# Performance work log

Measured on AMD Instinct MI355X. Metric: run time of the kernel, lower is better.

The kernel has to match this reference:

```python
import jax, jax.numpy as jnp
import numpy as np

N, D_IN, D_OUT = 4096, 1024, 1024


def setup_inputs() -> dict:
    key = jax.random.key(0)
    kx, kq, kk, kv = jax.random.split(key, 4)
    s = 1.0 / np.sqrt(D_IN)
    return {
        "x": jax.random.normal(kx, (N, D_IN), dtype=jnp.float32),
        "Wq": jax.random.normal(kq, (D_OUT, D_IN), dtype=jnp.float32) * s,
        "Wk": jax.random.normal(kk, (D_OUT, D_IN), dtype=jnp.float32) * s,
        "Wv": jax.random.normal(kv, (D_OUT, D_IN), dtype=jnp.float32) * s,
    }


def reference(x, Wq, Wk, Wv):
    # nn.Linear(d_in, d_out, bias=False): y = x @ W.T with W: [d_out, d_in]
    q = x @ Wq.T            # [N, d_out]
    k = x @ Wk.T            # [N, d_out]
    v = x @ Wv.T            # [N, d_out]
    scores = q @ k.T        # [N, N]
    scale = 1.0 / jnp.sqrt(jnp.asarray(k.shape[-1], dtype=x.dtype))
    attn = jax.nn.softmax(scores * scale, axis=-1)
    return attn @ v         # [N, d_out]
```

## Files before the change

kernel.cpp:

```cpp
#include <hip/hip_runtime.h>


typedef __attribute__((ext_vector_type(8))) __bf16 bf16x8;
typedef __attribute__((ext_vector_type(4))) float floatx4;

#define GLB_AS __attribute__((address_space(1)))
#define LDS_AS __attribute__((address_space(3)))

static __device__ __forceinline__ unsigned short f2bf_u16(float f) {
  union { float f; unsigned u; } x; x.f = f;
  unsigned r = x.u;
  r += 0x7fffu + ((r >> 16) & 1u);
  return (unsigned short)(r >> 16);
}
static __device__ __forceinline__ float bf2f(unsigned short u) {
  union { unsigned u; float f; } x; x.u = ((unsigned)u) << 16; return x.f;
}

__global__ __launch_bounds__(256) void cast_all(const float* __restrict__ x,
                                                const float* __restrict__ Wq,
                                                const float* __restrict__ Wk,
                                                const float* __restrict__ Wv,
                                                unsigned short* __restrict__ xb,
                                                unsigned short* __restrict__ wb) {
  const int i = blockIdx.x * 256 + threadIdx.x;
  const int NX4 = 4096 * 1024 / 4;
  const int NW4 = 1024 * 1024 / 4;
  const float* src; unsigned short* dst; int k;
  if (i < NX4)                { src = x;  dst = xb;                   k = i; }
  else if (i < NX4 + NW4)     { src = Wq; dst = wb;                   k = i - NX4; }
  else if (i < NX4 + 2 * NW4) { src = Wk; dst = wb + 1024 * 1024;     k = i - NX4 - NW4; }
  else                        { src = Wv; dst = wb + 2 * 1024 * 1024; k = i - NX4 - 2 * NW4; }
  float4 v = reinterpret_cast<const float4*>(src)[k];
  ushort4 o = make_ushort4(f2bf_u16(v.x), f2bf_u16(v.y), f2bf_u16(v.z), f2bf_u16(v.w));
  reinterpret_cast<ushort4*>(dst)[k] = o;
}

struct GemmOuts { void* c[4]; int ldc[4]; };

template <int EPI>
__global__ __launch_bounds__(256, 2) void gemm_bt(const unsigned short* __restrict__ A,
                                                  const unsigned short* __restrict__ B,
                                                  GemmOuts outs, int lda, int ldb,
                                                  int klen, float scale) {
  __shared__ unsigned short sh[24576];
  const int t = threadIdx.x;
  const int w = t >> 6, lane = t & 63;
  const int wm = w >> 1, wn = w & 1;
  const int gx = gridDim.x;
  const int nwg = gx * gridDim.y;
  int bid = blockIdx.y * gx + blockIdx.x;
  bid = (bid & 7) * (nwg >> 3) + (bid >> 3);
  const int row0 = (bid / gx) * 256;
  const int col0 = (bid % gx) * 128;
  const int z = blockIdx.z;
  const int kstart = z * klen;
  const int NT = klen >> 5;

  const int srow = t >> 2;
  const int scbe = (((t & 3) ^ ((t >> 3) & 3)) << 3);
  const unsigned short* gA0 = A + (size_t)(row0 + srow) * lda + kstart + scbe;
  const unsigned short* gA1 = gA0 + (size_t)64 * lda;
  const unsigned short* gA2 = gA0 + (size_t)128 * lda;
  const unsigned short* gA3 = gA0 + (size_t)192 * lda;
  const unsigned short* gB0 = B + (size_t)(col0 + srow) * ldb + kstart + scbe;
  const unsigned short* gB1 = gB0 + (size_t)64 * ldb;

#define STAGE(tl_) do { \
    const int bb_ = ((tl_) & 1) * 12288; \
    __builtin_amdgcn_global_load_lds((const GLB_AS void*)(gA0 + (tl_) * 32), \
        (LDS_AS void*)&sh[bb_ + t * 8], 16, 0, 0); \
    __builtin_amdgcn_global_load_lds((const GLB_AS void*)(gA1 + (tl_) * 32), \
        (LDS_AS void*)&sh[bb_ + 2048 + t * 8], 16, 0, 0); \
    __builtin_amdgcn_global_load_lds((const GLB_AS void*)(gA2 + (tl_) * 32), \
        (LDS_AS void*)&sh[bb_ + 4096 + t * 8], 16, 0, 0); \
    __builtin_amdgcn_global_load_lds((const GLB_AS void*)(gA3 + (tl_) * 32), \
        (LDS_AS void*)&sh[bb_ + 6144 + t * 8], 16, 0, 0); \
    __builtin_amdgcn_global_load_lds((const GLB_AS void*)(gB0 + (tl_) * 32), \
        (LDS_AS void*)&sh[bb_ + 8192 + t * 8], 16, 0, 0); \
    __builtin_amdgcn_global_load_lds((const GLB_AS void*)(gB1 + (tl_) * 32), \
        (LDS_AS void*)&sh[bb_ + 10240 + t * 8], 16, 0, 0); \
  } while (0)

  const int fr = lane & 15;
  const int sg = (((lane >> 4) ^ ((lane >> 1) & 3)) << 3);
  int aofs[8], bofs[4];
#pragma unroll
  for (int mf = 0; mf < 8; ++mf) aofs[mf] = ((wm * 128 + mf * 16 + fr) << 5) + sg;
#pragma unroll
  for (int nf = 0; nf < 4; ++nf) bofs[nf] = 8192 + ((wn * 64 + nf * 16 + fr) << 5) + sg;

  floatx4 acc[8][4] = {};

  STAGE(0);

  for (int tile = 0; tile < NT; ++tile) {
    if (tile + 1 < NT) {
      STAGE(tile + 1);
      asm volatile("s_waitcnt vmcnt(6)" ::: "memory");
    } else {
      asm volatile("s_waitcnt vmcnt(0)" ::: "memory");
    }
    __builtin_amdgcn_s_barrier();

    const int bo = (tile & 1) * 12288;
    bf16x8 af[8], bf[4];
#pragma unroll
    for (int mf = 0; mf < 8; ++mf) af[mf] = *(const bf16x8*)&sh[bo + aofs[mf]];
#pragma unroll
    for (int nf = 0; nf < 4; ++nf) bf[nf] = *(const bf16x8*)&sh[bo + bofs[nf]];
    __builtin_amdgcn_s_setprio(1);
#pragma unroll
    for (int mf = 0; mf < 8; ++mf)
#pragma unroll
      for (int nf = 0; nf < 4; ++nf)
        acc[mf][nf] = __builtin_amdgcn_mfma_f32_16x16x32_bf16(af[mf], bf[nf], acc[mf][nf], 0, 0, 0);
    __builtin_amdgcn_s_setprio(0);

    __builtin_amdgcn_s_barrier();
  }
#undef STAGE

  const int er = (lane >> 4) * 4;
  const int ec = lane & 15;

  if (EPI == 0) {
    unsigned short* Cb = (unsigned short*)outs.c[z];
    const int ldc = outs.ldc[z];
#pragma unroll
    for (int mf = 0; mf < 8; ++mf)
#pragma unroll
      for (int nf = 0; nf < 4; ++nf)
#pragma unroll
        for (int r = 0; r < 4; ++r)
          Cb[(size_t)(row0 + wm * 128 + mf * 16 + er + r) * ldc +
             (col0 + wn * 64 + nf * 16 + ec)] = f2bf_u16(acc[mf][nf][r] * scale);
  } else if (EPI == 2) {
    unsigned short* Pb = (unsigned short*)outs.c[0];
    float* rsp = (float*)outs.c[1];
    const int ldc = outs.ldc[0];
    const int rj = ((col0 >> 7) * 2 + wn) * 4096;
#pragma unroll
    for (int mf = 0; mf < 8; ++mf) {
#pragma unroll
      for (int r = 0; r < 4; ++r) {
        const int m = row0 + wm * 128 + mf * 16 + er + r;
        float rsum = 0.f;
#pragma unroll
        for (int nf = 0; nf < 4; ++nf) {
          const float e = __expf(acc[mf][nf][r] * scale);
          Pb[(size_t)m * ldc + (col0 + wn * 64 + nf * 16 + ec)] = f2bf_u16(e);
          rsum += e;
        }
        rsum += __shfl_xor(rsum, 1);
        rsum += __shfl_xor(rsum, 2);
        rsum += __shfl_xor(rsum, 4);
        rsum += __shfl_xor(rsum, 8);
        if (ec == 0) rsp[rj + m] = rsum;
      }
    }
  } else {
    if (col0 < 2048) {
      unsigned short* qkb = (unsigned short*)outs.c[0];
#pragma unroll
      for (int mf = 0; mf < 8; ++mf)
#pragma unroll
        for (int nf = 0; nf < 4; ++nf)
#pragma unroll
          for (int r = 0; r < 4; ++r)
            qkb[(size_t)(row0 + wm * 128 + mf * 16 + er + r) * 2048 +
                (col0 + wn * 64 + nf * 16 + ec)] = f2bf_u16(acc[mf][nf][r]);
    } else {
      unsigned short* vT = (unsigned short*)outs.c[1];
#pragma unroll
      for (int mf = 0; mf < 8; ++mf)
#pragma unroll
        for (int nf = 0; nf < 4; ++nf) {
          const int n = (col0 - 2048) + wn * 64 + nf * 16 + ec;
          const int mb = row0 + wm * 128 + mf * 16 + er;
          ushort4 o = make_ushort4(f2bf_u16(acc[mf][nf][0]), f2bf_u16(acc[mf][nf][1]),
                                   f2bf_u16(acc[mf][nf][2]), f2bf_u16(acc[mf][nf][3]));
          *reinterpret_cast<ushort4*>(&vT[(size_t)n * 4096 + mb]) = o;
        }
    }
  }
}

__global__ __launch_bounds__(256) void reduce_pv(float* __restrict__ out,
                                                 const unsigned short* __restrict__ p0,
                                                 const unsigned short* __restrict__ p1,
                                                 const float* __restrict__ rsp) {
  const int row = blockIdx.x;
  const int lane = threadIdx.x & 63;
  float s = rsp[lane * 4096 + row];
#pragma unroll
  for (int off = 32; off >= 1; off >>= 1) s += __shfl_xor(s, off);
  const float inv = 1.0f / s;
  const int idx = row * 256 + threadIdx.x;
  ushort4 a = ((const ushort4*)p0)[idx];
  ushort4 b = ((const ushort4*)p1)[idx];
  float4 o;
  o.x = (bf2f(a.x) + bf2f(b.x)) * inv;
  o.y = (bf2f(a.y) + bf2f(b.y)) * inv;
  o.z = (bf2f(a.z) + bf2f(b.z)) * inv;
  o.w = (bf2f(a.w) + bf2f(b.w)) * inv;
  ((float4*)out)[idx] = o;
}

extern "C" void kernel_launch(void* const* d_in, const int* in_sizes, int n_in,
                              void* d_out, int out_size, void* d_ws, size_t ws_size,
                              hipStream_t stream) {
  const float* x  = (const float*)d_in[0];
  const float* Wq = (const float*)d_in[1];
  const float* Wk = (const float*)d_in[2];
  const float* Wv = (const float*)d_in[3];
  float* out = (float*)d_out;

  const int N = 4096, D = 1024;

  char* ws = (char*)d_ws;
  unsigned short* P   = (unsigned short*)ws;
  unsigned short* qkb = (unsigned short*)(ws + (32u << 20));
  unsigned short* vT  = (unsigned short*)(ws + (48u << 20));
  unsigned short* xb  = (unsigned short*)(ws + (56u << 20));
  unsigned short* wb  = (unsigned short*)(ws + (64u << 20));
  float*          rsp = (float*)(ws + (70u << 20));
  unsigned short* p0  = xb;
  unsigned short* p1  = (unsigned short*)(ws + (72u << 20));

  cast_all<<<7168, 256, 0, stream>>>(x, Wq, Wk, Wv, xb, wb);

  GemmOuts oq; oq.c[0] = qkb; oq.c[1] = vT; oq.c[2] = oq.c[3] = qkb;
  oq.ldc[0] = 2048; oq.ldc[1] = 4096; oq.ldc[2] = oq.ldc[3] = 2048;
  gemm_bt<3><<<dim3(3 * D / 128, N / 256, 1), 256, 0, stream>>>(xb, wb, oq, D, D, D, 1.0f);

  GemmOuts os; os.c[0] = P; os.c[1] = rsp; os.c[2] = os.c[3] = P;
  os.ldc[0] = N; os.ldc[1] = 0; os.ldc[2] = os.ldc[3] = N;
  gemm_bt<2><<<dim3(N / 128, N / 256, 1), 256, 0, stream>>>(qkb, qkb + D, os, 2 * D, 2 * D, D, 0.03125f);

  GemmOuts op;
  op.c[0] = p0; op.ldc[0] = D;
  op.c[1] = p1; op.ldc[1] = D;
  op.c[2] = p0; op.ldc[2] = D;
  op.c[3] = p1; op.ldc[3] = D;
  gemm_bt<0><<<dim3(D / 128, N / 256, 2), 256, 0, stream>>>(P, vT, op, N, N, N / 2, 1.0f);

  reduce_pv<<<N, 256, 0, stream>>>(out, p0, p1, rsp);
}
```

Baseline: 141.7 us.

## Fuse fp32-to-bf16 input cast into QKV projection GEMM

Removes the separate cast kernel and has a dedicated QKV GEMM read fp32 x and weights directly, converting to bf16 with packed converts while staging into LDS. This saves a kernel launch and the write and reread of the bf16 copies of x and the weights. In exchange the GEMM reads fp32 data, twice the bytes per tile, and x is re-read and re-converted by each of the 24 column blocks. The prefetch is held in registers, which raises register pressure.

```diff
diff --git a/kernel.cpp b/kernel.cpp
--- a/kernel.cpp
+++ b/kernel.cpp
@@ -16,24 +16,10 @@
 static __device__ __forceinline__ float bf2f(unsigned short u) {
   union { unsigned u; float f; } x; x.u = ((unsigned)u) << 16; return x.f;
 }
-
-__global__ __launch_bounds__(256) void cast_all(const float* __restrict__ x,
-                                                const float* __restrict__ Wq,
-                                                const float* __restrict__ Wk,
-                                                const float* __restrict__ Wv,
-                                                unsigned short* __restrict__ xb,
-                                                unsigned short* __restrict__ wb) {
-  const int i = blockIdx.x * 256 + threadIdx.x;
-  const int NX4 = 4096 * 1024 / 4;
-  const int NW4 = 1024 * 1024 / 4;
-  const float* src; unsigned short* dst; int k;
-  if (i < NX4)                { src = x;  dst = xb;                   k = i; }
-  else if (i < NX4 + NW4)     { src = Wq; dst = wb;                   k = i - NX4; }
-  else if (i < NX4 + 2 * NW4) { src = Wk; dst = wb + 1024 * 1024;     k = i - NX4 - NW4; }
-  else                        { src = Wv; dst = wb + 2 * 1024 * 1024; k = i - NX4 - 2 * NW4; }
-  float4 v = reinterpret_cast<const float4*>(src)[k];
-  ushort4 o = make_ushort4(f2bf_u16(v.x), f2bf_u16(v.y), f2bf_u16(v.z), f2bf_u16(v.w));
-  reinterpret_cast<ushort4*>(dst)[k] = o;
+static __device__ __forceinline__ unsigned cvt_pk_bf16(float lo, float hi) {
+  unsigned r;
+  asm("v_cvt_pk_bf16_f32 %0, %1, %2" : "=v"(r) : "v"(lo), "v"(hi));
+  return r;
 }
 
 struct GemmOuts { void* c[4]; int ldc[4]; };
@@ -135,7 +121,7 @@
         for (int r = 0; r < 4; ++r)
           Cb[(size_t)(row0 + wm * 128 + mf * 16 + er + r) * ldc +
              (col0 + wn * 64 + nf * 16 + ec)] = f2bf_u16(acc[mf][nf][r] * scale);
-  } else if (EPI == 2) {
+  } else {
     unsigned short* Pb = (unsigned short*)outs.c[0];
     float* rsp = (float*)outs.c[1];
     const int ldc = outs.ldc[0];
@@ -159,30 +145,120 @@
         if (ec == 0) rsp[rj + m] = rsum;
       }
     }
+  }
+}
+
+__global__ __launch_bounds__(256, 2) void gemm_qkv(const float* __restrict__ X,
+                                                   const float* __restrict__ Wq,
+                                                   const float* __restrict__ Wk,
+                                                   const float* __restrict__ Wv,
+                                                   unsigned short* __restrict__ qkb,
+                                                   unsigned short* __restrict__ vT) {
+  __shared__ unsigned short sh[24576];
+  const int t = threadIdx.x;
+  const int w = t >> 6, lane = t & 63;
+  const int wm = w >> 1, wn = w & 1;
+  const int gx = gridDim.x;
+  const int nwg = gx * gridDim.y;
+  int bid = blockIdx.y * gx + blockIdx.x;
+  bid = (bid & 7) * (nwg >> 3) + (bid >> 3);
+  const int row0 = (bid / gx) * 256;
+  const int col0 = (bid % gx) * 128;
+  const float* Wsel = col0 < 1024 ? Wq : (col0 < 2048 ? Wk : Wv);
+  const int brow = col0 & 1023;
+  const int NT = 32;
+
+  const int srow = t >> 2;
+  const int scbe = (((t & 3) ^ ((t >> 3) & 3)) << 3);
+  const float* gA = X + (size_t)(row0 + srow) * 1024 + scbe;
+  const float* gB = Wsel + (size_t)(brow + srow) * 1024 + scbe;
+
+  float4 ra[12];
+#define LOADF(kt_) do { \
+    _Pragma("unroll") for (int r_ = 0; r_ < 4; ++r_) { \
+      const float* p_ = gA + (size_t)(r_ * 64) * 1024 + (kt_); \
+      ra[2 * r_]     = *(const float4*)p_; \
+      ra[2 * r_ + 1] = *(const float4*)(p_ + 4); } \
+    _Pragma("unroll") for (int r_ = 0; r_ < 2; ++r_) { \
+      const float* p_ = gB + (size_t)(r_ * 64) * 1024 + (kt_); \
+      ra[8 + 2 * r_] = *(const float4*)p_; \
+      ra[9 + 2 * r_] = *(const float4*)(p_ + 4); } \
+  } while (0)
+#define WRITELDS(bb_) do { \
+    _Pragma("unroll") for (int r_ = 0; r_ < 6; ++r_) { \
+      uint4 pk_; \
+      pk_.x = cvt_pk_bf16(ra[2 * r_].x,     ra[2 * r_].y); \
+      pk_.y = cvt_pk_bf16(ra[2 * r_].z,     ra[2 * r_].w); \
+      pk_.z = cvt_pk_bf16(ra[2 * r_ + 1].x, ra[2 * r_ + 1].y); \
+      pk_.w = cvt_pk_bf16(ra[2 * r_ + 1].z, ra[2 * r_ + 1].w); \
+      *(uint4*)&sh[(bb_) + r_ * 2048 + t * 8] = pk_; } \
+  } while (0)
+
+  const int fr = lane & 15;
+  const int sg = (((lane >> 4) ^ ((lane >> 1) & 3)) << 3);
+  int aofs[8], bofs[4];
+#pragma unroll
+  for (int mf = 0; mf < 8; ++mf) aofs[mf] = ((wm * 128 + mf * 16 + fr) << 5) + sg;
+#pragma unroll
+  for (int nf = 0; nf < 4; ++nf) bofs[nf] = 8192 + ((wn * 64 + nf * 16 + fr) << 5) + sg;
+
+  floatx4 acc[8][4] = {};
+
+  LOADF(0);
+  asm volatile("s_waitcnt vmcnt(0)" ::: "memory");
+  WRITELDS(0);
+  LOADF(32);
+  asm volatile("s_waitcnt lgkmcnt(0)" ::: "memory");
+  __builtin_amdgcn_s_barrier();
+
+  for (int tile = 0; tile < NT; ++tile) {
+    const int bo = (tile & 1) * 12288;
+    bf16x8 af[8], bf[4];
+#pragma unroll
+    for (int mf = 0; mf < 8; ++mf) af[mf] = *(const bf16x8*)&sh[bo + aofs[mf]];
+#pragma unroll
+    for (int nf = 0; nf < 4; ++nf) bf[nf] = *(const bf16x8*)&sh[bo + bofs[nf]];
+    __builtin_amdgcn_s_setprio(1);
+#pragma unroll
+    for (int mf = 0; mf < 8; ++mf)
+#pragma unroll
+      for (int nf = 0; nf < 4; ++nf)
+        acc[mf][nf] = __builtin_amdgcn_mfma_f32_16x16x32_bf16(af[mf], bf[nf], acc[mf][nf], 0, 0, 0);
+    __builtin_amdgcn_s_setprio(0);
+
+    if (tile + 1 < NT) {
+      asm volatile("s_waitcnt vmcnt(0)" ::: "memory");
+      WRITELDS(((tile + 1) & 1) * 12288);
+      if (tile + 2 < NT) LOADF((tile + 2) * 32);
+    }
+    asm volatile("s_waitcnt lgkmcnt(0)" ::: "memory");
+    __builtin_amdgcn_s_barrier();
+  }
+#undef LOADF
+#undef WRITELDS
+
+  const int er = (lane >> 4) * 4;
+  const int ec = lane & 15;
+  if (col0 < 2048) {
+#pragma unroll
+    for (int mf = 0; mf < 8; ++mf)
+#pragma unroll
+      for (int nf = 0; nf < 4; ++nf)
+#pragma unroll
+        for (int r = 0; r < 4; ++r)
+          qkb[(size_t)(row0 + wm * 128 + mf * 16 + er + r) * 2048 +
+              (col0 + wn * 64 + nf * 16 + ec)] = f2bf_u16(acc[mf][nf][r]);
   } else {
-    if (col0 < 2048) {
-      unsigned short* qkb = (unsigned short*)outs.c[0];
-#pragma unroll
-      for (int mf = 0; mf < 8; ++mf)
-#pragma unroll
-        for (int nf = 0; nf < 4; ++nf)
-#pragma unroll
-          for (int r = 0; r < 4; ++r)
-            qkb[(size_t)(row0 + wm * 128 + mf * 16 + er + r) * 2048 +
-                (col0 + wn * 64 + nf * 16 + ec)] = f2bf_u16(acc[mf][nf][r]);
-    } else {
-      unsigned short* vT = (unsigned short*)outs.c[1];
-#pragma unroll
-      for (int mf = 0; mf < 8; ++mf)
-#pragma unroll
-        for (int nf = 0; nf < 4; ++nf) {
-          const int n = (col0 - 2048) + wn * 64 + nf * 16 + ec;
-          const int mb = row0 + wm * 128 + mf * 16 + er;
-          ushort4 o = make_ushort4(f2bf_u16(acc[mf][nf][0]), f2bf_u16(acc[mf][nf][1]),
-                                   f2bf_u16(acc[mf][nf][2]), f2bf_u16(acc[mf][nf][3]));
-          *reinterpret_cast<ushort4*>(&vT[(size_t)n * 4096 + mb]) = o;
-        }
-    }
+#pragma unroll
+    for (int mf = 0; mf < 8; ++mf)
+#pragma unroll
+      for (int nf = 0; nf < 4; ++nf) {
+        const int n = (col0 - 2048) + wn * 64 + nf * 16 + ec;
+        const int mb = row0 + wm * 128 + mf * 16 + er;
+        ushort4 o = make_ushort4(f2bf_u16(acc[mf][nf][0]), f2bf_u16(acc[mf][nf][1]),
+                                 f2bf_u16(acc[mf][nf][2]), f2bf_u16(acc[mf][nf][3]));
+        *reinterpret_cast<ushort4*>(&vT[(size_t)n * 4096 + mb]) = o;
+      }
   }
 }
 
@@ -222,17 +298,11 @@
   unsigned short* P   = (unsigned short*)ws;
   unsigned short* qkb = (unsigned short*)(ws + (32u << 20));
   unsigned short* vT  = (unsigned short*)(ws + (48u << 20));
-  unsigned short* xb  = (unsigned short*)(ws + (56u << 20));
-  unsigned short* wb  = (unsigned short*)(ws + (64u << 20));
+  unsigned short* p0  = (unsigned short*)(ws + (56u << 20));
   float*          rsp = (float*)(ws + (70u << 20));
-  unsigned short* p0  = xb;
   unsigned short* p1  = (unsigned short*)(ws + (72u << 20));
 
-  cast_all<<<7168, 256, 0, stream>>>(x, Wq, Wk, Wv, xb, wb);
-
-  GemmOuts oq; oq.c[0] = qkb; oq.c[1] = vT; oq.c[2] = oq.c[3] = qkb;
-  oq.ldc[0] = 2048; oq.ldc[1] = 4096; oq.ldc[2] = oq.ldc[3] = 2048;
-  gemm_bt<3><<<dim3(3 * D / 128, N / 256, 1), 256, 0, stream>>>(xb, wb, oq, D, D, D, 1.0f);
+  gemm_qkv<<<dim3(3 * D / 128, N / 256, 1), 256, 0, stream>>>(x, Wq, Wk, Wv, qkb, vT);
 
   GemmOuts os; os.c[0] = P; os.c[1] = rsp; os.c[2] = os.c[3] = P;
   os.ldc[0] = N; os.ldc[1] = 0; os.ldc[2] = os.ldc[3] = N;
```

Measured after the change: 144.1 us. About the same (+1.6%).

## Fuse split-K PV reduction and normalization into GEMM epilogue via atomics

Applied to the files above, without the earlier changes.

Removes the final reduce_pv kernel and its bf16 partial buffers. The PV GEMM epilogue now divides each accumulator by the row sum and atomically adds fp32 results straight into a zeroed output. A small collapse_rs kernel precomputes row sums, and a memset clears the output. This trades one launch plus the partial-buffer write and read traffic for scattered fp32 atomics on a 4M-element output and an extra memset and launch.

```diff
diff --git a/kernel.cpp b/kernel.cpp
--- a/kernel.cpp
+++ b/kernel.cpp
@@ -12,9 +12,6 @@
   unsigned r = x.u;
   r += 0x7fffu + ((r >> 16) & 1u);
   return (unsigned short)(r >> 16);
-}
-static __device__ __forceinline__ float bf2f(unsigned short u) {
-  union { unsigned u; float f; } x; x.u = ((unsigned)u) << 16; return x.f;
 }
 
 __global__ __launch_bounds__(256) void cast_all(const float* __restrict__ x,
@@ -34,6 +31,15 @@
   float4 v = reinterpret_cast<const float4*>(src)[k];
   ushort4 o = make_ushort4(f2bf_u16(v.x), f2bf_u16(v.y), f2bf_u16(v.z), f2bf_u16(v.w));
   reinterpret_cast<ushort4*>(dst)[k] = o;
+}
+
+__global__ __launch_bounds__(256) void collapse_rs(const float* __restrict__ rsp,
+                                                   float* __restrict__ rs) {
+  const int r = blockIdx.x * 256 + threadIdx.x;
+  float s = 0.f;
+#pragma unroll
+  for (int j = 0; j < 64; ++j) s += rsp[j * 4096 + r];
+  rs[r] = s;
 }
 
 struct GemmOuts { void* c[4]; int ldc[4]; };
@@ -125,16 +131,21 @@
   const int ec = lane & 15;
 
   if (EPI == 0) {
-    unsigned short* Cb = (unsigned short*)outs.c[z];
-    const int ldc = outs.ldc[z];
-#pragma unroll
-    for (int mf = 0; mf < 8; ++mf)
-#pragma unroll
-      for (int nf = 0; nf < 4; ++nf)
-#pragma unroll
-        for (int r = 0; r < 4; ++r)
-          Cb[(size_t)(row0 + wm * 128 + mf * 16 + er + r) * ldc +
-             (col0 + wn * 64 + nf * 16 + ec)] = f2bf_u16(acc[mf][nf][r] * scale);
+    float* Of = (float*)outs.c[0];
+    const float* rsv = (const float*)outs.c[1];
+#pragma unroll
+    for (int mf = 0; mf < 8; ++mf) {
+#pragma unroll
+      for (int r = 0; r < 4; ++r) {
+        const int m = row0 + wm * 128 + mf * 16 + er + r;
+        const float inv = 1.0f / rsv[m];
+#pragma unroll
+        for (int nf = 0; nf < 4; ++nf) {
+          const int n = col0 + wn * 64 + nf * 16 + ec;
+          atomicAdd(&Of[(size_t)m * 1024 + n], acc[mf][nf][r] * inv);
+        }
+      }
+    }
   } else if (EPI == 2) {
     unsigned short* Pb = (unsigned short*)outs.c[0];
     float* rsp = (float*)outs.c[1];
@@ -186,27 +197,6 @@
   }
 }
 
-__global__ __launch_bounds__(256) void reduce_pv(float* __restrict__ out,
-                                                 const unsigned short* __restrict__ p0,
-                                                 const unsigned short* __restrict__ p1,
-                                                 const float* __restrict__ rsp) {
-  const int row = blockIdx.x;
-  const int lane = threadIdx.x & 63;
-  float s = rsp[lane * 4096 + row];
-#pragma unroll
-  for (int off = 32; off >= 1; off >>= 1) s += __shfl_xor(s, off);
-  const float inv = 1.0f / s;
-  const int idx = row * 256 + threadIdx.x;
-  ushort4 a = ((const ushort4*)p0)[idx];
-  ushort4 b = ((const ushort4*)p1)[idx];
-  float4 o;
-  o.x = (bf2f(a.x) + bf2f(b.x)) * inv;
-  o.y = (bf2f(a.y) + bf2f(b.y)) * inv;
-  o.z = (bf2f(a.z) + bf2f(b.z)) * inv;
-  o.w = (bf2f(a.w) + bf2f(b.w)) * inv;
-  ((float4*)out)[idx] = o;
-}
-
 extern "C" void kernel_launch(void* const* d_in, const int* in_sizes, int n_in,
                               void* d_out, int out_size, void* d_ws, size_t ws_size,
                               hipStream_t stream) {
@@ -225,8 +215,9 @@
   unsigned short* xb  = (unsigned short*)(ws + (56u << 20));
   unsigned short* wb  = (unsigned short*)(ws + (64u << 20));
   float*          rsp = (float*)(ws + (70u << 20));
-  unsigned short* p0  = xb;
-  unsigned short* p1  = (unsigned short*)(ws + (72u << 20));
+  float*          rs  = (float*)(ws + (71u << 20));
+
+  hipMemsetAsync(out, 0, (size_t)out_size * sizeof(float), stream);
 
   cast_all<<<7168, 256, 0, stream>>>(x, Wq, Wk, Wv, xb, wb);
 
@@ -238,12 +229,9 @@
   os.ldc[0] = N; os.ldc[1] = 0; os.ldc[2] = os.ldc[3] = N;
   gemm_bt<2><<<dim3(N / 128, N / 256, 1), 256, 0, stream>>>(qkb, qkb + D, os, 2 * D, 2 * D, D, 0.03125f);
 
-  GemmOuts op;
-  op.c[0] = p0; op.ldc[0] = D;
-  op.c[1] = p1; op.ldc[1] = D;
-  op.c[2] = p0; op.ldc[2] = D;
-  op.c[3] = p1; op.ldc[3] = D;
+  collapse_rs<<<16, 256, 0, stream>>>(rsp, rs);
+
+  GemmOuts op; op.c[0] = out; op.c[1] = rs; op.c[2] = op.c[3] = out;
+  op.ldc[0] = D; op.ldc[1] = 0; op.ldc[2] = op.ldc[3] = D;
   gemm_bt<0><<<dim3(D / 128, N / 256, 2), 256, 0, stream>>>(P, vT, op, N, N, N / 2, 1.0f);
-
-  reduce_pv<<<N, 256, 0, stream>>>(out, p0, p1, rsp);
-}
+}
```

Result: slower. 179.3 us (+26.5%).

## Use 256x256-tile 8-wave pingpong GEMM kernel for QK^T scores with exp epilogue

Applied to the files above, without the earlier changes.

Replaces the scores GEMM (q@k^T with the exp/row-sum epilogue) with a dedicated 512-thread kernel that computes 256x256 output tiles, double-buffers 64-wide K slices in 128 KB of LDS, and interleaves async global-to-LDS loads with MFMA phases under barriers and raised wave priority. The larger tile raises arithmetic intensity, and the staged schedule is meant to hide load latency. The row-sum partials now come from 64-column slices, so the rsp layout uses index (col0>>6)+wn, which matches the earlier per-64-column indexing. The large LDS footprint limits occupancy, and the many barriers add synchronisation cost.

```diff
diff --git a/kernel.cpp b/kernel.cpp
--- a/kernel.cpp
+++ b/kernel.cpp
@@ -34,6 +34,137 @@
   float4 v = reinterpret_cast<const float4*>(src)[k];
   ushort4 o = make_ushort4(f2bf_u16(v.x), f2bf_u16(v.y), f2bf_u16(v.z), f2bf_u16(v.w));
   reinterpret_cast<ushort4*>(dst)[k] = o;
+}
+
+__global__ __launch_bounds__(512, 2) void gemm8p_s(const unsigned short* __restrict__ A,
+                                                   const unsigned short* __restrict__ B,
+                                                   unsigned short* __restrict__ Pb,
+                                                   float* __restrict__ rsp,
+                                                   int lda, int ldb, int ldc,
+                                                   float scale) {
+  __shared__ unsigned short sh[65536];
+  const int t = threadIdx.x;
+  const int w = t >> 6, lane = t & 63;
+  const int wm = w >> 2, wn = w & 3;
+  const int gx = gridDim.x;
+  const int nwg = gx * gridDim.y;
+  int bid = blockIdx.y * gx + blockIdx.x;
+  bid = (bid & 7) * (nwg >> 3) + (bid >> 3);
+  const int row0 = (bid / gx) * 256;
+  const int col0 = (bid % gx) * 256;
+  const int NT = 16, NI = 8;
+
+  const int scol = (((t & 7) ^ ((t >> 4) & 7)) << 3);
+  const unsigned short* gA = A + (size_t)(row0 + (t >> 3)) * lda + scol;
+  const unsigned short* gB = B + (size_t)(col0 + (t >> 3)) * ldb + scol;
+
+#define STG(op_, h_, d_, tl_) do { \
+    const unsigned short* s0_ = (op_ ? gB : gA) + \
+        (size_t)((h_) * 128) * (op_ ? ldb : lda) + (tl_) * 64; \
+    const unsigned short* s1_ = s0_ + (size_t)64 * (op_ ? ldb : lda); \
+    unsigned short* l0_ = &sh[(d_) * 32768 + (op_) * 16384 + (h_) * 8192 + t * 8]; \
+    __builtin_amdgcn_global_load_lds((const GLB_AS void*)s0_, (LDS_AS void*)l0_, 16, 0, 0); \
+    __builtin_amdgcn_global_load_lds((const GLB_AS void*)s1_, (LDS_AS void*)(l0_ + 4096), 16, 0, 0); \
+  } while (0)
+
+  const int fr = lane & 15;
+  const int lh = lane >> 4;
+  const int key = (fr >> 1) & 7;
+  const int g0 = ((0 * 4 + lh) ^ key) << 3;
+  const int g1 = ((1 * 4 + lh) ^ key) << 3;
+
+  floatx4 acc[8][4] = {};
+  bf16x8 afr[4][2], bfr0[2][2], bfr1[2][2];
+
+#define RDA(d_, mh_) do { \
+    _Pragma("unroll") for (int mf = 0; mf < 4; ++mf) { \
+      const int rb_ = (d_) * 32768 + wm * 8192 + (((mh_) * 64 + mf * 16 + fr) << 6); \
+      afr[mf][0] = *(const bf16x8*)&sh[rb_ + g0]; \
+      afr[mf][1] = *(const bf16x8*)&sh[rb_ + g1]; } \
+  } while (0)
+#define RDB(d_, nh_, dst_) do { \
+    _Pragma("unroll") for (int nf = 0; nf < 2; ++nf) { \
+      const int rb_ = (d_) * 32768 + 16384 + (wn >> 1) * 8192 + \
+                      ((((wn & 1) * 64 + (nh_) * 32 + nf * 16 + fr)) << 6); \
+      dst_[nf][0] = *(const bf16x8*)&sh[rb_ + g0]; \
+      dst_[nf][1] = *(const bf16x8*)&sh[rb_ + g1]; } \
+  } while (0)
+#define MFMA16(mh_, nh_, bsrc_) do { \
+    __builtin_amdgcn_s_setprio(1); \
+    _Pragma("unroll") for (int mf = 0; mf < 4; ++mf) \
+      _Pragma("unroll") for (int nf = 0; nf < 2; ++nf) { \
+        acc[(mh_)*4+mf][(nh_)*2+nf] = __builtin_amdgcn_mfma_f32_16x16x32_bf16(afr[mf][0], bsrc_[nf][0], acc[(mh_)*4+mf][(nh_)*2+nf], 0, 0, 0); \
+        acc[(mh_)*4+mf][(nh_)*2+nf] = __builtin_amdgcn_mfma_f32_16x16x32_bf16(afr[mf][1], bsrc_[nf][1], acc[(mh_)*4+mf][(nh_)*2+nf], 0, 0, 0); } \
+    __builtin_amdgcn_s_setprio(0); \
+  } while (0)
+#define BAR()  __builtin_amdgcn_s_barrier()
+#define LGKM() do { asm volatile("s_waitcnt lgkmcnt(0)" ::: "memory"); \
+                    __builtin_amdgcn_sched_barrier(0); } while (0)
+
+  STG(1, 0, 0, 0); STG(0, 0, 0, 0); STG(1, 1, 0, 0); STG(0, 1, 0, 0);
+  STG(1, 0, 1, 1); STG(0, 0, 1, 1);
+  asm volatile("s_waitcnt vmcnt(4)" ::: "memory");
+  BAR();
+
+  for (int j = 0; j < NI; ++j) {
+    const bool more = (j < NI - 1);
+    RDA(0, 0); RDB(0, 0, bfr0);
+    STG(1, 1, 1, 2 * j + 1);
+    BAR(); LGKM(); MFMA16(0, 0, bfr0); BAR();
+    RDB(0, 1, bfr1);
+    STG(0, 1, 1, 2 * j + 1);
+    BAR(); LGKM(); MFMA16(0, 1, bfr1); BAR();
+    RDA(0, 1);
+    if (more) STG(1, 0, 0, 2 * j + 2);
+    BAR(); LGKM(); MFMA16(1, 0, bfr0); BAR();
+    if (more) STG(0, 0, 0, 2 * j + 2);
+    BAR(); LGKM(); MFMA16(1, 1, bfr1);
+    if (j == NI - 1) { asm volatile("s_waitcnt vmcnt(0)" ::: "memory"); }
+    else             { asm volatile("s_waitcnt vmcnt(4)" ::: "memory"); }
+    BAR();
+    RDA(1, 0); RDB(1, 0, bfr0);
+    if (more) STG(1, 1, 0, 2 * j + 2);
+    BAR(); LGKM(); MFMA16(0, 0, bfr0); BAR();
+    RDB(1, 1, bfr1);
+    if (more) STG(0, 1, 0, 2 * j + 2);
+    BAR(); LGKM(); MFMA16(0, 1, bfr1); BAR();
+    RDA(1, 1);
+    if (more) STG(1, 0, 1, 2 * j + 3);
+    BAR(); LGKM(); MFMA16(1, 0, bfr0); BAR();
+    if (more) STG(0, 0, 1, 2 * j + 3);
+    BAR(); LGKM(); MFMA16(1, 1, bfr1);
+    asm volatile("s_waitcnt vmcnt(4)" ::: "memory");
+    BAR();
+  }
+#undef STG
+#undef RDA
+#undef RDB
+#undef MFMA16
+#undef BAR
+#undef LGKM
+
+  const int er = (lane >> 4) * 4;
+  const int ec = lane & 15;
+  const int rj = ((col0 >> 6) + wn) * 4096;
+#pragma unroll
+  for (int ai = 0; ai < 8; ++ai) {
+#pragma unroll
+    for (int r = 0; r < 4; ++r) {
+      const int m = row0 + wm * 128 + (ai >> 2) * 64 + (ai & 3) * 16 + er + r;
+      float rsum = 0.f;
+#pragma unroll
+      for (int bj = 0; bj < 4; ++bj) {
+        const float e = __expf(acc[ai][bj][r] * scale);
+        Pb[(size_t)m * ldc + (col0 + wn * 64 + (bj >> 1) * 32 + (bj & 1) * 16 + ec)] = f2bf_u16(e);
+        rsum += e;
+      }
+      rsum += __shfl_xor(rsum, 1);
+      rsum += __shfl_xor(rsum, 2);
+      rsum += __shfl_xor(rsum, 4);
+      rsum += __shfl_xor(rsum, 8);
+      if (ec == 0) rsp[rj + m] = rsum;
+    }
+  }
 }
 
 struct GemmOuts { void* c[4]; int ldc[4]; };
@@ -135,30 +266,6 @@
         for (int r = 0; r < 4; ++r)
           Cb[(size_t)(row0 + wm * 128 + mf * 16 + er + r) * ldc +
              (col0 + wn * 64 + nf * 16 + ec)] = f2bf_u16(acc[mf][nf][r] * scale);
-  } else if (EPI == 2) {
-    unsigned short* Pb = (unsigned short*)outs.c[0];
-    float* rsp = (float*)outs.c[1];
-    const int ldc = outs.ldc[0];
-    const int rj = ((col0 >> 7) * 2 + wn) * 4096;
-#pragma unroll
-    for (int mf = 0; mf < 8; ++mf) {
-#pragma unroll
-      for (int r = 0; r < 4; ++r) {
-        const int m = row0 + wm * 128 + mf * 16 + er + r;
-        float rsum = 0.f;
-#pragma unroll
-        for (int nf = 0; nf < 4; ++nf) {
-          const float e = __expf(acc[mf][nf][r] * scale);
-          Pb[(size_t)m * ldc + (col0 + wn * 64 + nf * 16 + ec)] = f2bf_u16(e);
-          rsum += e;
-        }
-        rsum += __shfl_xor(rsum, 1);
-        rsum += __shfl_xor(rsum, 2);
-        rsum += __shfl_xor(rsum, 4);
-        rsum += __shfl_xor(rsum, 8);
-        if (ec == 0) rsp[rj + m] = rsum;
-      }
-    }
   } else {
     if (col0 < 2048) {
       unsigned short* qkb = (unsigned short*)outs.c[0];
@@ -234,9 +341,8 @@
   oq.ldc[0] = 2048; oq.ldc[1] = 4096; oq.ldc[2] = oq.ldc[3] = 2048;
   gemm_bt<3><<<dim3(3 * D / 128, N / 256, 1), 256, 0, stream>>>(xb, wb, oq, D, D, D, 1.0f);
 
-  GemmOuts os; os.c[0] = P; os.c[1] = rsp; os.c[2] = os.c[3] = P;
-  os.ldc[0] = N; os.ldc[1] = 0; os.ldc[2] = os.ldc[3] = N;
-  gemm_bt<2><<<dim3(N / 128, N / 256, 1), 256, 0, stream>>>(qkb, qkb + D, os, 2 * D, 2 * D, D, 0.03125f);
+  gemm8p_s<<<dim3(N / 256, N / 256, 1), 512, 0, stream>>>(qkb, qkb + D, P, rsp,
+                                                          2 * D, 2 * D, N, 0.03125f);
 
   GemmOuts op;
   op.c[0] = p0; op.ldc[0] = D;
```

Result: faster. 138.1 us (-2.6%).
